# Performance work log

Measured on AMD Instinct MI355X. Metric: run time of the kernel, lower is better.

The kernel has to match this reference:

```python
import jax, jax.numpy as jnp
import numpy as np

N_NODES = 50000
N_EDGES = 800000
SIZES = [128, 256, 256, 128]
EPS = 1e-5


def setup_inputs() -> dict:
    key = jax.random.key(0)
    ks = jax.random.split(key, 2 + 5 * (len(SIZES) - 1))
    inp = {
        "x": jax.random.normal(ks[0], (N_NODES, SIZES[0]), dtype=jnp.float32),
        "edge_index": jax.random.randint(ks[1], (2, N_EDGES), 0, N_NODES, dtype=jnp.int64),
    }
    k = 2
    for i, (fin, fout) in enumerate(zip(SIZES[:-1], SIZES[1:])):
        scale = 1.0 / np.sqrt(fin)
        inp[f"W{i}"] = jax.random.normal(ks[k], (fout, fin), dtype=jnp.float32) * scale; k += 1
        inp[f"b{i}"] = jnp.zeros((fout,), dtype=jnp.float32)
        inp[f"g{i}"] = jnp.ones((fout,), dtype=jnp.float32)   # LayerNorm weight
        inp[f"be{i}"] = jnp.zeros((fout,), dtype=jnp.float32)  # LayerNorm bias
        inp[f"a{i}"] = jnp.full((1,), 0.25, dtype=jnp.float32)  # PReLU slope
        k += 3  # keep key consumption deterministic
    return inp


def _gcn_conv(x, src, dst, dinv, W, b):
    # GCNConv: h = x @ W^T; aggregate norm(src,dst) * h[src] into dst; add bias.
    h = x @ W.T  # [N, F_out]
    norm = dinv[src] * dinv[dst]  # [E+N]
    msg = norm[:, None] * h[src]  # [E+N, F_out]
    return jax.ops.segment_sum(msg, dst, num_segments=N_NODES) + b


def _layernorm_graph(x, g, be):
    # PyG LayerNorm(mode='graph'): normalize over all nodes and channels.
    mu = x.mean()
    xc = x - mu
    var = (xc * xc).mean()
    return xc / jnp.sqrt(var + EPS) * g + be


def _prelu(x, a):
    return jnp.where(x >= 0, x, a * x)


def reference(x, edge_index, W0, b0, g0, be0, a0, W1, b1, g1, be1, a1, W2, b2, g2, be2, a2):
    loop = jnp.arange(N_NODES, dtype=edge_index.dtype)
    src = jnp.concatenate([edge_index[0], loop])  # add self-loops
    dst = jnp.concatenate([edge_index[1], loop])
    deg = jax.ops.segment_sum(jnp.ones_like(dst, dtype=x.dtype), dst, num_segments=N_NODES)
    dinv = jax.lax.rsqrt(deg)  # deg >= 1 due to self-loops
    params = [(W0, b0, g0, be0, a0), (W1, b1, g1, be1, a1), (W2, b2, g2, be2, a2)]
    for W, b, g, be, a in params:
        x = _gcn_conv(x, src, dst, dinv, W, b)
        x = _layernorm_graph(x, g, be)
        x = _prelu(x, a)
    return x
```

## Files before the change

### kernel.cpp

```cpp
#include <hip/hip_runtime.h>

#define N_NODES 50000
#define N_EDGES 800000
#define EPS 1e-5f

typedef __attribute__((ext_vector_type(8))) short bf16x8;
typedef __attribute__((ext_vector_type(4))) float f32x4;
typedef __attribute__((ext_vector_type(4))) unsigned short us4;

__device__ __forceinline__ unsigned short f2b(float f) {
    union { float f; unsigned int u; } v; v.f = f;
    unsigned int r = v.u + 0x7fffu + ((v.u >> 16) & 1u);
    return (unsigned short)(r >> 16);
}
__device__ __forceinline__ float b2f(unsigned short b) {
    union { unsigned int u; float f; } v; v.u = ((unsigned int)b) << 16;
    return v.f;
}


#define RED_BUCKETS 64
#define RED_FLOATS_PER_LAYER (RED_BUCKETS * 16)


#define CV_NX (N_NODES * 128 / 4)
#define CV_N0 (256 * 128 / 4)
#define CV_N1 (256 * 256 / 4)
#define CV_N2 (128 * 256 / 4)

__global__ void prep_kernel(const float* __restrict__ x0, const float* __restrict__ W0,
                            const float* __restrict__ W1, const float* __restrict__ W2,
                            unsigned short* __restrict__ xb, unsigned short* __restrict__ wb0,
                            unsigned short* __restrict__ wb1, unsigned short* __restrict__ wb2,
                            int* __restrict__ deg, int* __restrict__ fill,
                            int* __restrict__ hist, float* __restrict__ red) {
    int i = blockIdx.x * 256 + threadIdx.x;
    if (i < N_NODES) { deg[i] = 0; fill[i] = 0; }
    if (i < 256) hist[i] = 0;
    if (i < 3 * RED_FLOATS_PER_LAYER) red[i] = 0.f;
    int j = i;
    if (j < CV_NX) {
        float4 v = reinterpret_cast<const float4*>(x0)[j];
        int n = j >> 5;
        int col0 = (j & 31) * 4;
        us4 o;
        o[0] = f2b(v.x); o[1] = f2b(v.y); o[2] = f2b(v.z); o[3] = f2b(v.w);
        *reinterpret_cast<us4*>(xb + ((size_t)(col0 >> 5) * N_NODES + n) * 32 + (col0 & 31)) = o;
        return;
    }
    const float* s;
    unsigned short* d;
    if ((j -= CV_NX) < CV_N0) { s = W0; d = wb0; }
    else if ((j -= CV_N0) < CV_N1) { s = W1; d = wb1; }
    else if ((j -= CV_N1) < CV_N2) { s = W2; d = wb2; }
    else return;
    float4 v = reinterpret_cast<const float4*>(s)[j];
    us4 o;
    o[0] = f2b(v.x); o[1] = f2b(v.y); o[2] = f2b(v.z); o[3] = f2b(v.w);
    reinterpret_cast<us4*>(d)[j] = o;
}


__global__ void count_kernel(const int* __restrict__ dst, int* __restrict__ deg, int e) {
    for (int i = blockIdx.x * blockDim.x + threadIdx.x; i < e; i += gridDim.x * blockDim.x)
        atomicAdd(&deg[dst[i]], 1);
}

__global__ void scan1_kernel(const int* __restrict__ deg, float* __restrict__ dinv,
                             int* __restrict__ bsum, int* __restrict__ hist, int n) {
    __shared__ int lh[256];
    lh[threadIdx.x] = 0;
    __syncthreads();
    int i = blockIdx.x * 256 + threadIdx.x;
    int v = (i < n) ? deg[i] : 0;
    if (i < n) {
        dinv[i] = rsqrtf((float)(v + 1));
        atomicAdd(&lh[v < 255 ? v : 255], 1);
    }
    int t = v;
    #pragma unroll
    for (int off = 1; off < 64; off <<= 1) t += __shfl_xor(t, off);
    __shared__ int wsum[4];
    int wid = threadIdx.x >> 6, lane = threadIdx.x & 63;
    if (lane == 0) wsum[wid] = t;
    __syncthreads();
    if (threadIdx.x == 0) bsum[blockIdx.x] = wsum[0] + wsum[1] + wsum[2] + wsum[3];
    if (lh[threadIdx.x] > 0) atomicAdd(&hist[threadIdx.x], lh[threadIdx.x]);
}

__global__ void scan2_kernel(const int* __restrict__ bsum, int* __restrict__ bpre, int nb,
                             const int* __restrict__ hist, int* __restrict__ binfill) {
    __shared__ int sm[256];
    int t = threadIdx.x;
    sm[t] = (t < nb) ? bsum[t] : 0;
    __syncthreads();
    #pragma unroll
    for (int d = 1; d < 256; d <<= 1) {
        int x = (t >= d) ? sm[t - d] : 0;
        __syncthreads();
        sm[t] += x;
        __syncthreads();
    }
    bpre[t] = (t > 0) ? sm[t - 1] : 0;
    __syncthreads();
    sm[t] = hist[t];
    __syncthreads();
    #pragma unroll
    for (int d = 1; d < 256; d <<= 1) {
        int x = (t >= d) ? sm[t - d] : 0;
        __syncthreads();
        sm[t] += x;
        __syncthreads();
    }
    binfill[t] = (t > 0) ? sm[t - 1] : 0;
}

__global__ void scan3_kernel(const int* __restrict__ deg, const int* __restrict__ bpre,
                             int* __restrict__ off, int n) {
    __shared__ int sm[256];
    int t = threadIdx.x;
    int i = blockIdx.x * 256 + t;
    int v = (i < n) ? deg[i] : 0;
    sm[t] = v;
    __syncthreads();
    #pragma unroll
    for (int d = 1; d < 256; d <<= 1) {
        int x = (t >= d) ? sm[t - d] : 0;
        __syncthreads();
        sm[t] += x;
        __syncthreads();
    }
    if (i < n) off[i + 1] = sm[t] + bpre[blockIdx.x];
    if (i == 0) off[0] = 0;
}

__global__ void permute_kernel(const int* __restrict__ deg, int* __restrict__ binfill,
                               int* __restrict__ perm, int n) {
    __shared__ int lhist[256];
    __shared__ int lbase[256];
    int t = threadIdx.x;
    lhist[t] = 0;
    __syncthreads();
    int i = blockIdx.x * 256 + t;
    int b = 0, lpos = 0;
    bool act = i < n;
    if (act) {
        int v = deg[i];
        b = v < 255 ? v : 255;
        lpos = atomicAdd(&lhist[b], 1);
    }
    __syncthreads();
    if (lhist[t] > 0) lbase[t] = atomicAdd(&binfill[t], lhist[t]);
    __syncthreads();
    if (act) perm[lbase[b] + lpos] = i;
}

__global__ void scatter_kernel(const int* __restrict__ src, const int* __restrict__ dst,
                               const int* __restrict__ coff, int* __restrict__ fill,
                               const float* __restrict__ dinv,
                               unsigned int* __restrict__ epack, int e) {
    for (int i = blockIdx.x * blockDim.x + threadIdx.x; i < e; i += gridDim.x * blockDim.x) {
        int d = dst[i];
        int s = src[i];
        int pos = coff[d] + atomicAdd(&fill[d], 1);
        epack[pos] = ((unsigned int)f2b(dinv[s] * dinv[d]) << 16) | (unsigned int)s;
    }
}


template<int BN, bool TRANSFORM, bool ADD_BIAS, bool FUSE_RED>
__device__ __forceinline__ void gemm_body(
    const unsigned short* __restrict__ Xin, const unsigned short* __restrict__ Wb,
    const float* __restrict__ bias, const float* __restrict__ redin,
    const float* __restrict__ gw, const float* __restrict__ bw,
    const float* __restrict__ asl, float* __restrict__ redout,
    unsigned short* __restrict__ Hout, int M, int K, float inv_count) {
    constexpr int FR_N = BN / 64;
    __shared__ unsigned short xs[2][64 * 32];
    int tid = threadIdx.x;
    int wid = tid >> 6, lane = tid & 63;
    int l16 = lane & 15, kg = lane >> 4;
    int srow = tid >> 2, sblk = tid & 3;
    int m0 = blockIdx.x * 64;
    int colbase = wid * (BN / 4);

    float mu = 0.f, rstd = 0.f, alpha = 0.f;
    if (TRANSFORM) {
        float s = redin[lane * 16], s2 = redin[lane * 16 + 1];
        #pragma unroll
        for (int off = 1; off < 64; off <<= 1) { s += __shfl_xor(s, off); s2 += __shfl_xor(s2, off); }
        mu = s * inv_count;
        rstd = rsqrtf(s2 * inv_count - mu * mu + EPS);
        alpha = asl[0];
    }

    int gmr = m0 + srow;
    bool inm = (gmr < M);
    const unsigned short* xrow = Xin + (size_t)gmr * 32 + sblk * 8;
    unsigned short* xdst = &xs[0][srow * 32 + ((sblk ^ (srow & 3)) * 8)];

    auto stage = [&](int k0, int buf) {
        bf16x8 xv = {};
        if (inm) {
            bf16x8 u = *reinterpret_cast<const bf16x8*>(xrow + (size_t)(k0 >> 5) * N_NODES * 32);
            if (TRANSFORM) {
                int f0 = k0 + sblk * 8;
                float ga[8], ba[8];
                *reinterpret_cast<float4*>(&ga[0]) = *reinterpret_cast<const float4*>(gw + f0);
                *reinterpret_cast<float4*>(&ga[4]) = *reinterpret_cast<const float4*>(gw + f0 + 4);
                *reinterpret_cast<float4*>(&ba[0]) = *reinterpret_cast<const float4*>(bw + f0);
                *reinterpret_cast<float4*>(&ba[4]) = *reinterpret_cast<const float4*>(bw + f0 + 4);
                #pragma unroll
                for (int i = 0; i < 8; ++i) {
                    float A = rstd * ga[i];
                    float B = ba[i] - mu * A;
                    float v = fmaf(b2f((unsigned short)u[i]), A, B);
                    v = fmaf(fminf(v, 0.f), alpha - 1.0f, v);
                    xv[i] = (short)f2b(v);
                }
            } else {
                xv = u;
            }
        }
        *reinterpret_cast<bf16x8*>(xdst + buf * (64 * 32)) = xv;
    };

    stage(0, 0);
    f32x4 acc[4][FR_N] = {};
    int nsteps = K / 32;
    for (int s = 0; s < nsteps; ++s) {
        __syncthreads();
        int k0 = s * 32;
        if (s + 1 < nsteps) stage(k0 + 32, (s + 1) & 1);
        bf16x8 b[FR_N];
        #pragma unroll
        for (int j = 0; j < FR_N; ++j)
            b[j] = *reinterpret_cast<const bf16x8*>(
                Wb + (size_t)(colbase + j * 16 + l16) * K + k0 + kg * 8);
        const unsigned short* xbuf = xs[s & 1];
        bf16x8 a[4];
        #pragma unroll
        for (int i = 0; i < 4; ++i) {
            int ar = i * 16 + l16;
            a[i] = *reinterpret_cast<const bf16x8*>(xbuf + ar * 32 + ((kg ^ (ar & 3)) * 8));
        }
        #pragma unroll
        for (int i = 0; i < 4; ++i)
            #pragma unroll
            for (int j = 0; j < FR_N; ++j)
                acc[i][j] = __builtin_amdgcn_mfma_f32_16x16x32_bf16(b[j], a[i], acc[i][j], 0, 0, 0);
    }

    float bsel[FR_N][4];
    if (ADD_BIAS) {
        #pragma unroll
        for (int j = 0; j < FR_N; ++j)
            *reinterpret_cast<float4*>(bsel[j]) =
                *reinterpret_cast<const float4*>(bias + colbase + j * 16 + kg * 4);
    }
    float s = 0.f, s2 = 0.f;
    #pragma unroll
    for (int i = 0; i < 4; ++i) {
        int row = m0 + i * 16 + l16;
        if (row < M) {
            #pragma unroll
            for (int j = 0; j < FR_N; ++j) {
                int col = colbase + j * 16 + kg * 4;
                us4 o;
                #pragma unroll
                for (int r = 0; r < 4; ++r) {
                    float v = acc[i][j][r] + (ADD_BIAS ? bsel[j][r] : 0.f);
                    if (FUSE_RED) { s += v; s2 += v * v; }
                    o[r] = f2b(v);
                }
                *reinterpret_cast<us4*>(
                    Hout + ((size_t)(col >> 5) * N_NODES + row) * 32 + (col & 31)) = o;
            }
        }
    }
    if (FUSE_RED) {
        #pragma unroll
        for (int off = 1; off < 64; off <<= 1) { s += __shfl_xor(s, off); s2 += __shfl_xor(s2, off); }
        if (lane == 0) {
            int bkt = (blockIdx.x & (RED_BUCKETS - 1)) * 16;
            atomicAdd(&redout[bkt], s);
            atomicAdd(&redout[bkt + 1], s2);
        }
    }
}


template<int COLS, bool ADD_BIAS, bool FUSE_RED>
__device__ __forceinline__ void agg_body(
    const unsigned short* __restrict__ Hb, const int* __restrict__ coff,
    const unsigned int* __restrict__ epack, const float* __restrict__ dinv,
    const int* __restrict__ perm,
    const float* __restrict__ bias, unsigned short* __restrict__ Y,
    float* __restrict__ red) {
    constexpr int CHUNKS = COLS / 32;
    int chunk = blockIdx.x % CHUNKS;
    int nodeblk = blockIdx.x / CHUNKS;
    int t = threadIdx.x;
    int nidx = nodeblk * 64 + (t >> 2);
    int rl = t & 3;
    bool active = nidx < N_NODES;
    int node = 0;
    if (active) node = perm[nidx];
    const unsigned short* base = Hb + (size_t)chunk * N_NODES * 32 + rl * 8;
    int s0 = 0, s1 = 0;
    float wc = 0.f;
    if (active) {
        s0 = coff[node]; s1 = coff[node + 1];
        float di = dinv[node];
        wc = di * di;
    }
    float acc[8] = {};
    bf16x8 vc = {};
    bool have = active;
    if (have) vc = *reinterpret_cast<const bf16x8*>(base + (size_t)node * 32);
    unsigned int u1 = 0;
    if (active && s0 < s1) u1 = epack[s0];
    int k = s0 - 1;
    while (__any(have)) {
        int k1 = k + 1, k2 = k + 2;
        bool have1 = have && (k1 < s1);
        unsigned int u2 = 0;
        if (have && k2 < s1) u2 = epack[k2];
        float wn = 0.f;
        bf16x8 vn = {};
        if (have1) {
            wn = b2f((unsigned short)(u1 >> 16));
            vn = *reinterpret_cast<const bf16x8*>(base + (size_t)(u1 & 0xffffu) * 32);
        }
        if (have) {
            #pragma unroll
            for (int i = 0; i < 8; ++i) acc[i] += wc * b2f((unsigned short)vc[i]);
        }
        k = k1; wc = wn; vc = vn; u1 = u2; have = have1;
    }
    if (ADD_BIAS && active) {
        #pragma unroll
        for (int i = 0; i < 8; ++i) acc[i] += bias[chunk * 32 + rl * 8 + i];
    }
    if (FUSE_RED) {
        float s = 0.f, s2 = 0.f;
        #pragma unroll
        for (int i = 0; i < 8; ++i) { s += acc[i]; s2 += acc[i] * acc[i]; }
        #pragma unroll
        for (int off = 1; off < 64; off <<= 1) { s += __shfl_xor(s, off); s2 += __shfl_xor(s2, off); }
        if ((t & 63) == 0) {
            int bkt = (blockIdx.x & (RED_BUCKETS - 1)) * 16;
            atomicAdd(&red[bkt], s);
            atomicAdd(&red[bkt + 1], s2);
        }
    }
    if (active) {
        bf16x8 o;
        #pragma unroll
        for (int i = 0; i < 8; ++i) o[i] = (short)f2b(acc[i]);
        __builtin_nontemporal_store(
            o, reinterpret_cast<bf16x8*>(Y + ((size_t)chunk * N_NODES + node) * 32 + rl * 8));
    }
}


__global__ __launch_bounds__(256) void gemm_l0(const unsigned short* X, const unsigned short* W,
                                               const float* bias, float* redout,
                                               unsigned short* H, int M, int K, float ic) {
    gemm_body<256, false, true, true>(X, W, bias, nullptr, nullptr, nullptr, nullptr, redout, H, M, K, ic);
}
__global__ __launch_bounds__(256) void gemm_l1(const unsigned short* X, const unsigned short* W,
                                               const float* redin, const float* gw, const float* bw,
                                               const float* asl, unsigned short* H, int M, int K, float ic) {
    gemm_body<256, true, false, false>(X, W, nullptr, redin, gw, bw, asl, nullptr, H, M, K, ic);
}
__global__ __launch_bounds__(256) void gemm_l2(const unsigned short* X, const unsigned short* W,
                                               const float* redin, const float* gw, const float* bw,
                                               const float* asl, unsigned short* H, int M, int K, float ic) {
    gemm_body<128, true, false, false>(X, W, nullptr, redin, gw, bw, asl, nullptr, H, M, K, ic);
}
__global__ void agg_l0(const unsigned short* Hb, const int* coff, const unsigned int* ep,
                       const float* dinv, const int* perm, unsigned short* Y) {
    agg_body<128, false, false>(Hb, coff, ep, dinv, perm, nullptr, Y, nullptr);
}
__global__ void agg_l1(const unsigned short* Hb, const int* coff, const unsigned int* ep,
                       const float* dinv, const int* perm, const float* bias,
                       unsigned short* Y, float* red) {
    agg_body<256, true, true>(Hb, coff, ep, dinv, perm, bias, Y, red);
}
__global__ void agg_l2(const unsigned short* Hb, const int* coff, const unsigned int* ep,
                       const float* dinv, const int* perm, const float* bias,
                       unsigned short* Y, float* red) {
    agg_body<128, true, true>(Hb, coff, ep, dinv, perm, bias, Y, red);
}


__global__ void norm_final(const unsigned short* __restrict__ Yb, const float* __restrict__ red,
                           const float* __restrict__ g, const float* __restrict__ be,
                           const float* __restrict__ a, float* __restrict__ X,
                           float inv_count) {
    int lane = threadIdx.x & 63;
    float s = red[lane * 16], s2 = red[lane * 16 + 1];
    #pragma unroll
    for (int off = 1; off < 64; off <<= 1) { s += __shfl_xor(s, off); s2 += __shfl_xor(s2, off); }
    float mu = s * inv_count;
    float rstd = rsqrtf(s2 * inv_count - mu * mu + EPS);
    float alpha = a[0];
    int total = N_NODES * 128 / 8;
    for (int i = blockIdx.x * blockDim.x + threadIdx.x; i < total; i += gridDim.x * blockDim.x) {
        bf16x8 v = reinterpret_cast<const bf16x8*>(Yb)[i];
        int c = i / (N_NODES * 4);
        int rem = i - c * (N_NODES * 4);
        int n = rem >> 2;
        int r = rem & 3;
        int f0 = c * 32 + r * 8;
        float o[8];
        #pragma unroll
        for (int j = 0; j < 8; ++j) {
            float t = (b2f((unsigned short)v[j]) - mu) * rstd * g[f0 + j] + be[f0 + j];
            o[j] = t >= 0.f ? t : alpha * t;
        }
        float* xp = X + (size_t)n * 128 + f0;
        *reinterpret_cast<float4*>(xp) = make_float4(o[0], o[1], o[2], o[3]);
        *reinterpret_cast<float4*>(xp + 4) = make_float4(o[4], o[5], o[6], o[7]);
    }
}


extern "C" void kernel_launch(void* const* d_in, const int* in_sizes, int n_in,
                              void* d_out, int out_size, void* d_ws, size_t ws_size,
                              hipStream_t stream) {
    const float* x0 = (const float*)d_in[0];
    const int* ei = (const int*)d_in[1];
    const float* W[3] = {(const float*)d_in[2], (const float*)d_in[7], (const float*)d_in[12]};
    const float* bb[3] = {(const float*)d_in[3], (const float*)d_in[8], (const float*)d_in[13]};
    const float* gg[3] = {(const float*)d_in[4], (const float*)d_in[9], (const float*)d_in[14]};
    const float* be[3] = {(const float*)d_in[5], (const float*)d_in[10], (const float*)d_in[15]};
    const float* aa[3] = {(const float*)d_in[6], (const float*)d_in[11], (const float*)d_in[16]};

    char* ws = (char*)d_ws;
    size_t o = 0;
    auto alloc = [&](size_t bytes) {
        void* p = ws + o;
        o = (o + bytes + 255) & ~(size_t)255;
        return p;
    };
    int* deg = (int*)alloc(N_NODES * 4);
    int* fill = (int*)alloc(N_NODES * 4);
    int* coff = (int*)alloc((N_NODES + 1) * 4);
    unsigned int* epack = (unsigned int*)alloc((size_t)N_EDGES * 4);
    float* dinv = (float*)alloc(N_NODES * 4);
    int* bsum = (int*)alloc(256 * 4);
    int* bpre = (int*)alloc(256 * 4);
    int* hist = (int*)alloc(256 * 4);
    int* binfill = (int*)alloc(256 * 4);
    int* perm = (int*)alloc(N_NODES * 4);
    float* red = (float*)alloc(3 * RED_FLOATS_PER_LAYER * 4);
    unsigned short* Wb0 = (unsigned short*)alloc(256 * 128 * 2);
    unsigned short* Wb1 = (unsigned short*)alloc(256 * 256 * 2);
    unsigned short* Wb2 = (unsigned short*)alloc(128 * 256 * 2);
    unsigned short* xb = (unsigned short*)alloc((size_t)N_NODES * 128 * 2);
    unsigned short* hb = (unsigned short*)alloc((size_t)N_NODES * 256 * 2);
    unsigned short* yb = (unsigned short*)alloc((size_t)N_NODES * 256 * 2);

    const int* e_src = ei;
    const int* e_dst = ei + N_EDGES;
    int nb = (N_NODES + 255) / 256;

    int cvtot = CV_NX + CV_N0 + CV_N1 + CV_N2;
    prep_kernel<<<(cvtot + 255) / 256, 256, 0, stream>>>(x0, W[0], W[1], W[2], xb, Wb0, Wb1, Wb2,
                                                         deg, fill, hist, red);
    count_kernel<<<2048, 256, 0, stream>>>(e_dst, deg, N_EDGES);
    scan1_kernel<<<nb, 256, 0, stream>>>(deg, dinv, bsum, hist, N_NODES);
    scan2_kernel<<<1, 256, 0, stream>>>(bsum, bpre, nb, hist, binfill);
    scan3_kernel<<<nb, 256, 0, stream>>>(deg, bpre, coff, N_NODES);
    permute_kernel<<<nb, 256, 0, stream>>>(deg, binfill, perm, N_NODES);
    scatter_kernel<<<2048, 256, 0, stream>>>(e_src, e_dst, coff, fill, dinv, epack, N_EDGES);

    int gm = (N_NODES + 63) / 64;
    float ic256 = 1.0f / (N_NODES * 256.0f);
    float ic128 = 1.0f / (N_NODES * 128.0f);

    agg_l0<<<gm * 4, 256, 0, stream>>>(xb, coff, epack, dinv, perm, hb);
    gemm_l0<<<gm, 256, 0, stream>>>(hb, Wb0, bb[0], red + 0, yb, N_NODES, 128, ic256);

    gemm_l1<<<gm, 256, 0, stream>>>(yb, Wb1, red + 0, gg[0], be[0], aa[0], hb, N_NODES, 256, ic256);
    agg_l1<<<gm * 8, 256, 0, stream>>>(hb, coff, epack, dinv, perm, bb[1], yb,
                                       red + RED_FLOATS_PER_LAYER);

    gemm_l2<<<gm, 256, 0, stream>>>(yb, Wb2, red + RED_FLOATS_PER_LAYER, gg[1], be[1], aa[1], hb,
                                    N_NODES, 256, ic256);
    agg_l2<<<gm * 4, 256, 0, stream>>>(hb, coff, epack, dinv, perm, bb[2], yb,
                                       red + 2 * RED_FLOATS_PER_LAYER);

    norm_final<<<2048, 256, 0, stream>>>(yb, red + 2 * RED_FLOATS_PER_LAYER, gg[2], be[2], aa[2],
                                         (float*)d_out, ic128);
}
```

Before: 359.5 us.

## Relabel nodes in degree-sorted order so CSR offsets derive from histogram

Nodes are renumbered by degree bucket, and all feature buffers, edge sources and CSR offsets use the permuted index. Offsets then come straight from the degree histogram, which removes the per-node prefix-scan kernels. The aggregation kernels read contiguous rows with no perm indirection, and norm_final applies the inverse permutation when writing the output. This adds a permuted gather when converting x, inverse-permutation lookups in scatter, and a gathered read in the final normalisation.

```diff
diff --git a/kernel.cpp b/kernel.cpp
--- a/kernel.cpp
+++ b/kernel.cpp
@@ -22,16 +22,16 @@
 #define RED_BUCKETS 64
 #define RED_FLOATS_PER_LAYER (RED_BUCKETS * 16)
 
-
 #define CV_NX (N_NODES * 128 / 4)
 #define CV_N0 (256 * 128 / 4)
 #define CV_N1 (256 * 256 / 4)
 #define CV_N2 (128 * 256 / 4)
 
-__global__ void prep_kernel(const float* __restrict__ x0, const float* __restrict__ W0,
-                            const float* __restrict__ W1, const float* __restrict__ W2,
-                            unsigned short* __restrict__ xb, unsigned short* __restrict__ wb0,
-                            unsigned short* __restrict__ wb1, unsigned short* __restrict__ wb2,
+
+__global__ void prep_kernel(const float* __restrict__ W0, const float* __restrict__ W1,
+                            const float* __restrict__ W2,
+                            unsigned short* __restrict__ wb0, unsigned short* __restrict__ wb1,
+                            unsigned short* __restrict__ wb2,
                             int* __restrict__ deg, int* __restrict__ fill,
                             int* __restrict__ hist, float* __restrict__ red) {
     int i = blockIdx.x * 256 + threadIdx.x;
@@ -39,18 +39,9 @@
     if (i < 256) hist[i] = 0;
     if (i < 3 * RED_FLOATS_PER_LAYER) red[i] = 0.f;
     int j = i;
-    if (j < CV_NX) {
-        float4 v = reinterpret_cast<const float4*>(x0)[j];
-        int n = j >> 5;
-        int col0 = (j & 31) * 4;
-        us4 o;
-        o[0] = f2b(v.x); o[1] = f2b(v.y); o[2] = f2b(v.z); o[3] = f2b(v.w);
-        *reinterpret_cast<us4*>(xb + ((size_t)(col0 >> 5) * N_NODES + n) * 32 + (col0 & 31)) = o;
-        return;
-    }
     const float* s;
     unsigned short* d;
-    if ((j -= CV_NX) < CV_N0) { s = W0; d = wb0; }
+    if (j < CV_N0) { s = W0; d = wb0; }
     else if ((j -= CV_N0) < CV_N1) { s = W1; d = wb1; }
     else if ((j -= CV_N1) < CV_N2) { s = W2; d = wb2; }
     else return;
@@ -66,33 +57,27 @@
         atomicAdd(&deg[dst[i]], 1);
 }
 
-__global__ void scan1_kernel(const int* __restrict__ deg, float* __restrict__ dinv,
-                             int* __restrict__ bsum, int* __restrict__ hist, int n) {
+__global__ void histo_kernel(const int* __restrict__ deg, float* __restrict__ dinv,
+                             int* __restrict__ hist, int n) {
     __shared__ int lh[256];
     lh[threadIdx.x] = 0;
     __syncthreads();
     int i = blockIdx.x * 256 + threadIdx.x;
-    int v = (i < n) ? deg[i] : 0;
     if (i < n) {
+        int v = deg[i];
         dinv[i] = rsqrtf((float)(v + 1));
         atomicAdd(&lh[v < 255 ? v : 255], 1);
     }
-    int t = v;
-    #pragma unroll
-    for (int off = 1; off < 64; off <<= 1) t += __shfl_xor(t, off);
-    __shared__ int wsum[4];
-    int wid = threadIdx.x >> 6, lane = threadIdx.x & 63;
-    if (lane == 0) wsum[wid] = t;
-    __syncthreads();
-    if (threadIdx.x == 0) bsum[blockIdx.x] = wsum[0] + wsum[1] + wsum[2] + wsum[3];
+    __syncthreads();
     if (lh[threadIdx.x] > 0) atomicAdd(&hist[threadIdx.x], lh[threadIdx.x]);
 }
 
-__global__ void scan2_kernel(const int* __restrict__ bsum, int* __restrict__ bpre, int nb,
-                             const int* __restrict__ hist, int* __restrict__ binfill) {
+__global__ void scan2_kernel(const int* __restrict__ hist, int* __restrict__ binpre,
+                             int* __restrict__ binfill, int* __restrict__ edgepre) {
     __shared__ int sm[256];
     int t = threadIdx.x;
-    sm[t] = (t < nb) ? bsum[t] : 0;
+    int h = hist[t];
+    sm[t] = h;
     __syncthreads();
     #pragma unroll
     for (int d = 1; d < 256; d <<= 1) {
@@ -101,9 +86,11 @@
         sm[t] += x;
         __syncthreads();
     }
-    bpre[t] = (t > 0) ? sm[t - 1] : 0;
-    __syncthreads();
-    sm[t] = hist[t];
+    int npre = (t > 0) ? sm[t - 1] : 0;
+    binpre[t] = npre;
+    binfill[t] = npre;
+    __syncthreads();
+    sm[t] = h * t;
     __syncthreads();
     #pragma unroll
     for (int d = 1; d < 256; d <<= 1) {
@@ -112,30 +99,14 @@
         sm[t] += x;
         __syncthreads();
     }
-    binfill[t] = (t > 0) ? sm[t - 1] : 0;
-}
-
-__global__ void scan3_kernel(const int* __restrict__ deg, const int* __restrict__ bpre,
-                             int* __restrict__ off, int n) {
-    __shared__ int sm[256];
-    int t = threadIdx.x;
-    int i = blockIdx.x * 256 + t;
-    int v = (i < n) ? deg[i] : 0;
-    sm[t] = v;
-    __syncthreads();
-    #pragma unroll
-    for (int d = 1; d < 256; d <<= 1) {
-        int x = (t >= d) ? sm[t - d] : 0;
-        __syncthreads();
-        sm[t] += x;
-        __syncthreads();
-    }
-    if (i < n) off[i + 1] = sm[t] + bpre[blockIdx.x];
-    if (i == 0) off[0] = 0;
-}
-
-__global__ void permute_kernel(const int* __restrict__ deg, int* __restrict__ binfill,
-                               int* __restrict__ perm, int n) {
+    edgepre[t] = (t > 0) ? sm[t - 1] : 0;
+}
+
+__global__ void permute_kernel(const int* __restrict__ deg, const float* __restrict__ dinv,
+                               const int* __restrict__ binpre, int* __restrict__ binfill,
+                               const int* __restrict__ edgepre,
+                               int* __restrict__ perm, int* __restrict__ iperm,
+                               float* __restrict__ dinv2s, int* __restrict__ soff, int n) {
     __shared__ int lhist[256];
     __shared__ int lbase[256];
     int t = threadIdx.x;
@@ -152,18 +123,41 @@
     __syncthreads();
     if (lhist[t] > 0) lbase[t] = atomicAdd(&binfill[t], lhist[t]);
     __syncthreads();
-    if (act) perm[lbase[b] + lpos] = i;
+    if (act) {
+        int p = lbase[b] + lpos;
+        perm[p] = i;
+        iperm[i] = p;
+        float di = dinv[i];
+        dinv2s[p] = di * di;
+        soff[p] = edgepre[b] + (p - binpre[b]) * b;
+    }
+    if (blockIdx.x == 0 && t == 0) soff[n] = N_EDGES;
+}
+
+__global__ void convert_x_kernel(const float* __restrict__ x0, const int* __restrict__ perm,
+                                 unsigned short* __restrict__ xb) {
+    int j = blockIdx.x * 256 + threadIdx.x;
+    if (j >= CV_NX) return;
+    int p = j >> 5;
+    int c4 = j & 31;
+    int orig = perm[p];
+    float4 v = reinterpret_cast<const float4*>(x0)[orig * 32 + c4];
+    int col0 = c4 * 4;
+    us4 o;
+    o[0] = f2b(v.x); o[1] = f2b(v.y); o[2] = f2b(v.z); o[3] = f2b(v.w);
+    *reinterpret_cast<us4*>(xb + ((size_t)(col0 >> 5) * N_NODES + p) * 32 + (col0 & 31)) = o;
 }
 
 __global__ void scatter_kernel(const int* __restrict__ src, const int* __restrict__ dst,
-                               const int* __restrict__ coff, int* __restrict__ fill,
-                               const float* __restrict__ dinv,
+                               const int* __restrict__ soff, int* __restrict__ fill,
+                               const float* __restrict__ dinv, const int* __restrict__ iperm,
                                unsigned int* __restrict__ epack, int e) {
     for (int i = blockIdx.x * blockDim.x + threadIdx.x; i < e; i += gridDim.x * blockDim.x) {
         int d = dst[i];
         int s = src[i];
-        int pos = coff[d] + atomicAdd(&fill[d], 1);
-        epack[pos] = ((unsigned int)f2b(dinv[s] * dinv[d]) << 16) | (unsigned int)s;
+        int pd = iperm[d];
+        int pos = soff[pd] + atomicAdd(&fill[pd], 1);
+        epack[pos] = ((unsigned int)f2b(dinv[s] * dinv[d]) << 16) | (unsigned int)iperm[s];
     }
 }
 
@@ -292,32 +286,28 @@
 
 template<int COLS, bool ADD_BIAS, bool FUSE_RED>
 __device__ __forceinline__ void agg_body(
-    const unsigned short* __restrict__ Hb, const int* __restrict__ coff,
-    const unsigned int* __restrict__ epack, const float* __restrict__ dinv,
-    const int* __restrict__ perm,
+    const unsigned short* __restrict__ Hb, const int* __restrict__ soff,
+    const unsigned int* __restrict__ epack, const float* __restrict__ dinv2s,
     const float* __restrict__ bias, unsigned short* __restrict__ Y,
     float* __restrict__ red) {
     constexpr int CHUNKS = COLS / 32;
     int chunk = blockIdx.x % CHUNKS;
     int nodeblk = blockIdx.x / CHUNKS;
     int t = threadIdx.x;
-    int nidx = nodeblk * 64 + (t >> 2);
+    int p = nodeblk * 64 + (t >> 2);
     int rl = t & 3;
-    bool active = nidx < N_NODES;
-    int node = 0;
-    if (active) node = perm[nidx];
+    bool active = p < N_NODES;
     const unsigned short* base = Hb + (size_t)chunk * N_NODES * 32 + rl * 8;
     int s0 = 0, s1 = 0;
     float wc = 0.f;
     if (active) {
-        s0 = coff[node]; s1 = coff[node + 1];
-        float di = dinv[node];
-        wc = di * di;
+        s0 = soff[p]; s1 = soff[p + 1];
+        wc = dinv2s[p];
     }
     float acc[8] = {};
     bf16x8 vc = {};
     bool have = active;
-    if (have) vc = *reinterpret_cast<const bf16x8*>(base + (size_t)node * 32);
+    if (have) vc = *reinterpret_cast<const bf16x8*>(base + (size_t)p * 32);
     unsigned int u1 = 0;
     if (active && s0 < s1) u1 = epack[s0];
     int k = s0 - 1;
@@ -359,7 +349,7 @@
         #pragma unroll
         for (int i = 0; i < 8; ++i) o[i] = (short)f2b(acc[i]);
         __builtin_nontemporal_store(
-            o, reinterpret_cast<bf16x8*>(Y + ((size_t)chunk * N_NODES + node) * 32 + rl * 8));
+            o, reinterpret_cast<bf16x8*>(Y + ((size_t)chunk * N_NODES + p) * 32 + rl * 8));
     }
 }
 
@@ -379,23 +369,22 @@
                                                const float* asl, unsigned short* H, int M, int K, float ic) {
     gemm_body<128, true, false, false>(X, W, nullptr, redin, gw, bw, asl, nullptr, H, M, K, ic);
 }
-__global__ void agg_l0(const unsigned short* Hb, const int* coff, const unsigned int* ep,
-                       const float* dinv, const int* perm, unsigned short* Y) {
-    agg_body<128, false, false>(Hb, coff, ep, dinv, perm, nullptr, Y, nullptr);
-}
-__global__ void agg_l1(const unsigned short* Hb, const int* coff, const unsigned int* ep,
-                       const float* dinv, const int* perm, const float* bias,
-                       unsigned short* Y, float* red) {
-    agg_body<256, true, true>(Hb, coff, ep, dinv, perm, bias, Y, red);
-}
-__global__ void agg_l2(const unsigned short* Hb, const int* coff, const unsigned int* ep,
-                       const float* dinv, const int* perm, const float* bias,
-                       unsigned short* Y, float* red) {
-    agg_body<128, true, true>(Hb, coff, ep, dinv, perm, bias, Y, red);
-}
-
-
-__global__ void norm_final(const unsigned short* __restrict__ Yb, const float* __restrict__ red,
+__global__ void agg_l0(const unsigned short* Hb, const int* soff, const unsigned int* ep,
+                       const float* dinv2s, unsigned short* Y) {
+    agg_body<128, false, false>(Hb, soff, ep, dinv2s, nullptr, Y, nullptr);
+}
+__global__ void agg_l1(const unsigned short* Hb, const int* soff, const unsigned int* ep,
+                       const float* dinv2s, const float* bias, unsigned short* Y, float* red) {
+    agg_body<256, true, true>(Hb, soff, ep, dinv2s, bias, Y, red);
+}
+__global__ void agg_l2(const unsigned short* Hb, const int* soff, const unsigned int* ep,
+                       const float* dinv2s, const float* bias, unsigned short* Y, float* red) {
+    agg_body<128, true, true>(Hb, soff, ep, dinv2s, bias, Y, red);
+}
+
+
+__global__ void norm_final(const unsigned short* __restrict__ Yb, const int* __restrict__ iperm,
+                           const float* __restrict__ red,
                            const float* __restrict__ g, const float* __restrict__ be,
                            const float* __restrict__ a, float* __restrict__ X,
                            float inv_count) {
@@ -406,14 +395,14 @@
     float mu = s * inv_count;
     float rstd = rsqrtf(s2 * inv_count - mu * mu + EPS);
     float alpha = a[0];
-    int total = N_NODES * 128 / 8;
+    int total = N_NODES * 16;
     for (int i = blockIdx.x * blockDim.x + threadIdx.x; i < total; i += gridDim.x * blockDim.x) {
-        bf16x8 v = reinterpret_cast<const bf16x8*>(Yb)[i];
-        int c = i / (N_NODES * 4);
-        int rem = i - c * (N_NODES * 4);
-        int n = rem >> 2;
-        int r = rem & 3;
-        int f0 = c * 32 + r * 8;
+        int n = i >> 4;
+        int r = i & 15;
+        int f0 = r * 8;
+        int p = iperm[n];
+        bf16x8 v = *reinterpret_cast<const bf16x8*>(
+            Yb + ((size_t)(f0 >> 5) * N_NODES + p) * 32 + (f0 & 31));
         float o[8];
         #pragma unroll
         for (int j = 0; j < 8; ++j) {
@@ -447,14 +436,16 @@
     };
     int* deg = (int*)alloc(N_NODES * 4);
     int* fill = (int*)alloc(N_NODES * 4);
-    int* coff = (int*)alloc((N_NODES + 1) * 4);
+    int* soff = (int*)alloc((N_NODES + 1) * 4);
     unsigned int* epack = (unsigned int*)alloc((size_t)N_EDGES * 4);
     float* dinv = (float*)alloc(N_NODES * 4);
-    int* bsum = (int*)alloc(256 * 4);
-    int* bpre = (int*)alloc(256 * 4);
+    float* dinv2s = (float*)alloc(N_NODES * 4);
     int* hist = (int*)alloc(256 * 4);
+    int* binpre = (int*)alloc(256 * 4);
     int* binfill = (int*)alloc(256 * 4);
+    int* edgepre = (int*)alloc(256 * 4);
     int* perm = (int*)alloc(N_NODES * 4);
+    int* iperm = (int*)alloc(N_NODES * 4);
     float* red = (float*)alloc(3 * RED_FLOATS_PER_LAYER * 4);
     unsigned short* Wb0 = (unsigned short*)alloc(256 * 128 * 2);
     unsigned short* Wb1 = (unsigned short*)alloc(256 * 256 * 2);
@@ -467,32 +458,32 @@
     const int* e_dst = ei + N_EDGES;
     int nb = (N_NODES + 255) / 256;
 
-    int cvtot = CV_NX + CV_N0 + CV_N1 + CV_N2;
-    prep_kernel<<<(cvtot + 255) / 256, 256, 0, stream>>>(x0, W[0], W[1], W[2], xb, Wb0, Wb1, Wb2,
-                                                         deg, fill, hist, red);
+    prep_kernel<<<nb, 256, 0, stream>>>(W[0], W[1], W[2], Wb0, Wb1, Wb2, deg, fill, hist, red);
     count_kernel<<<2048, 256, 0, stream>>>(e_dst, deg, N_EDGES);
-    scan1_kernel<<<nb, 256, 0, stream>>>(deg, dinv, bsum, hist, N_NODES);
-    scan2_kernel<<<1, 256, 0, stream>>>(bsum, bpre, nb, hist, binfill);
-    scan3_kernel<<<nb, 256, 0, stream>>>(deg, bpre, coff, N_NODES);
-    permute_kernel<<<nb, 256, 0, stream>>>(deg, binfill, perm, N_NODES);
-    scatter_kernel<<<2048, 256, 0, stream>>>(e_src, e_dst, coff, fill, dinv, epack, N_EDGES);
+    histo_kernel<<<nb, 256, 0, stream>>>(deg, dinv, hist, N_NODES);
+    scan2_kernel<<<1, 256, 0, stream>>>(hist, binpre, binfill, edgepre);
+    permute_kernel<<<nb, 256, 0, stream>>>(deg, dinv, binpre, binfill, edgepre,
+                                           perm, iperm, dinv2s, soff, N_NODES);
+    convert_x_kernel<<<(CV_NX + 255) / 256, 256, 0, stream>>>(x0, perm, xb);
+    scatter_kernel<<<2048, 256, 0, stream>>>(e_src, e_dst, soff, fill, dinv, iperm,
+                                             epack, N_EDGES);
 
     int gm = (N_NODES + 63) / 64;
     float ic256 = 1.0f / (N_NODES * 256.0f);
     float ic128 = 1.0f / (N_NODES * 128.0f);
 
-    agg_l0<<<gm * 4, 256, 0, stream>>>(xb, coff, epack, dinv, perm, hb);
+    agg_l0<<<gm * 4, 256, 0, stream>>>(xb, soff, epack, dinv2s, hb);
     gemm_l0<<<gm, 256, 0, stream>>>(hb, Wb0, bb[0], red + 0, yb, N_NODES, 128, ic256);
 
     gemm_l1<<<gm, 256, 0, stream>>>(yb, Wb1, red + 0, gg[0], be[0], aa[0], hb, N_NODES, 256, ic256);
-    agg_l1<<<gm * 8, 256, 0, stream>>>(hb, coff, epack, dinv, perm, bb[1], yb,
+    agg_l1<<<gm * 8, 256, 0, stream>>>(hb, soff, epack, dinv2s, bb[1], yb,
                                        red + RED_FLOATS_PER_LAYER);
 
     gemm_l2<<<gm, 256, 0, stream>>>(yb, Wb2, red + RED_FLOATS_PER_LAYER, gg[1], be[1], aa[1], hb,
                                     N_NODES, 256, ic256);
-    agg_l2<<<gm * 4, 256, 0, stream>>>(hb, coff, epack, dinv, perm, bb[2], yb,
+    agg_l2<<<gm * 4, 256, 0, stream>>>(hb, soff, epack, dinv2s, bb[2], yb,
                                        red + 2 * RED_FLOATS_PER_LAYER);
 
-    norm_final<<<2048, 256, 0, stream>>>(yb, red + 2 * RED_FLOATS_PER_LAYER, gg[2], be[2], aa[2],
-                                         (float*)d_out, ic128);
-}
+    norm_final<<<2048, 256, 0, stream>>>(yb, iperm, red + 2 * RED_FLOATS_PER_LAYER,
+                                         gg[2], be[2], aa[2], (float*)d_out, ic128);
+}
```

Result: faster. 323.1 us (-10.1%).
